# Kernel optimization log

Hardware: AMD Instinct MI355X
Metric: run time of the kernel (lower is better)

The kernel has to match this reference:

```python
import jax, jax.numpy as jnp
import numpy as np

BETA = 0.25      # commitment loss weight
DECAY = 0.99     # EMA decay
EPS = 1e-5       # Laplace smoothing for counts


def setup_inputs() -> dict:
    key = jax.random.key(0)
    k1, k2, k3 = jax.random.split(key, 3)
    B, d, h, w, K = 16, 64, 64, 64, 1024
    z_e = jax.random.normal(k1, (B, d, h, w), dtype=jnp.float32)
    codebook = jax.random.normal(k2, (K, d), dtype=jnp.float32)
    ema_count = jnp.ones((K,), dtype=jnp.float32)
    ema_sum = jax.random.normal(k3, (K, d), dtype=jnp.float32)
    return {"z_e": z_e, "codebook": codebook, "ema_count": ema_count, "ema_sum": ema_sum}


def reference(z_e, codebook, ema_count, ema_sum):
    B, d, h, w = z_e.shape
    K = codebook.shape[0]
    # [B,d,h,w] -> [N,d], N = B*h*w
    z_flat = jnp.transpose(z_e, (0, 2, 3, 1)).reshape(-1, d)
    # squared euclidean distances [N,K]
    dist = (jnp.sum(z_flat * z_flat, axis=1, keepdims=True)
            - 2.0 * (z_flat @ codebook.T)
            + jnp.sum(codebook * codebook, axis=1)[None, :])
    indices = jnp.argmin(dist, axis=1)                      # [N] int
    e_k = codebook[indices].reshape(B, h, w, d).transpose(0, 3, 1, 2)  # [B,d,h,w]

    # --- EMA codebook update (training mode, no grad) ---
    zf = jax.lax.stop_gradient(z_flat)
    counts = jax.ops.segment_sum(jnp.ones((zf.shape[0],), dtype=zf.dtype), indices, num_segments=K)
    sums = jax.ops.segment_sum(zf, indices, num_segments=K)
    new_count = ema_count * DECAY + (1.0 - DECAY) * counts
    new_sum = ema_sum * DECAY + (1.0 - DECAY) * sums
    n = jnp.sum(new_count)
    count_s = (new_count + EPS) / (n + K * EPS) * n
    new_codebook = new_sum / count_s[:, None]

    # straight-through estimator
    e_k_ste = z_e + jax.lax.stop_gradient(e_k - z_e)
    L_commit = (jnp.mean((z_e - jax.lax.stop_gradient(e_k)) ** 2)
                + BETA * jnp.mean((jax.lax.stop_gradient(z_e) - e_k) ** 2))
    return (e_k_ste, indices.reshape(B, h, w), L_commit, new_codebook, new_count, new_sum)
```

## Files before the change

### kernel.cpp

```cpp
#include <hip/hip_runtime.h>
#include <hip/hip_bf16.h>
#include <hip/hip_fp16.h>

#define NB 16
#define DD 64
#define HW 4096
#define NTOT 65536
#define KC 1024

#define O_EK   0
#define O_IDX  4194304
#define O_L    4259840
#define O_CB   4259841
#define O_CNT  4325377
#define O_SUM  4326401

#define WS_IDX    0
#define WS_LCPART 65536
#define WS_N      66048
#define WS_CNORM  66560
#define WS_PSUM   67584
#define WS_PCNT   329728
#define WS_CBH    399360
#define WS_CBL    432128

typedef _Float16 v8h __attribute__((ext_vector_type(8)));
typedef float    v4f __attribute__((ext_vector_type(4)));
typedef unsigned short ush;

__global__ __launch_bounds__(256) void k_pre(const float* __restrict__ cb,
                                             const float* __restrict__ ema_count,
                                             float* __restrict__ cnorm,
                                             float* __restrict__ n_ws,
                                             unsigned short* __restrict__ cbh,
                                             unsigned short* __restrict__ cbl) {
    const int t = threadIdx.x;
    const int w = (blockIdx.x * 256 + t) >> 6;
    const int l = t & 63;
    float s = 0.f;
    if (l < 16) {
        float4 v = *(const float4*)(cb + (size_t)w * DD + l * 4);
        s = v.x * v.x + v.y * v.y + v.z * v.z + v.w * v.w;
    }
#pragma unroll
    for (int m = 1; m <= 8; m <<= 1) s += __shfl_xor(s, m, 64);
    if (l == 0) cnorm[w] = s;

    const int e4 = blockIdx.x * 256 + t;
    if (e4 < 16384) {
        float4 v4 = ((const float4*)cb)[e4];
        __half hx = __float2half(v4.x), hy = __float2half(v4.y),
               hz = __float2half(v4.z), hw2 = __float2half(v4.w);
        ushort4 h4 = { __half_as_ushort(hx), __half_as_ushort(hy),
                       __half_as_ushort(hz), __half_as_ushort(hw2) };
        ((ushort4*)cbh)[e4] = h4;
        ushort4 l4 = { __half_as_ushort(__float2half(v4.x - __half2float(hx))),
                       __half_as_ushort(__float2half(v4.y - __half2float(hy))),
                       __half_as_ushort(__float2half(v4.z - __half2float(hz))),
                       __half_as_ushort(__float2half(v4.w - __half2float(hw2))) };
        ((ushort4*)cbl)[e4] = l4;
    }

    if (blockIdx.x == 0) {
        __shared__ float red[256];
        red[t] = ema_count[t] + ema_count[t + 256] + ema_count[t + 512] + ema_count[t + 768];
        __syncthreads();
        for (int s2 = 128; s2 >= 1; s2 >>= 1) {
            if (t < s2) red[t] += red[t + s2];
            __syncthreads();
        }
        if (t == 0) n_ws[0] = 0.99f * red[0] + 0.01f * 65536.0f;
    }
}

__global__ __launch_bounds__(512) void k_argmin(const float* __restrict__ z_e,
                                                const float* __restrict__ cbf,
                                                const unsigned short* __restrict__ cbh,
                                                const unsigned short* __restrict__ cbl,
                                                const float* __restrict__ cnorm,
                                                int* __restrict__ idx_ws,
                                                float* __restrict__ out) {
    __shared__ __align__(16) unsigned char ldsAB[32768];
    __shared__ __align__(16) float slab[2048];
    __shared__ int idx_lds[128];
    __shared__ int flagrows[128];
    __shared__ int flagi1[128];
    __shared__ int flagi2[128];
    __shared__ int nflag;

    ush (*A2h)[128][8]  = (ush(*)[128][8])(ldsAB);
    ush (*A2l)[128][8]  = (ush(*)[128][8])(ldsAB + 16384);
    ush (*B2h)[8][64][8] = (ush(*)[8][64][8])(ldsAB);
    ush (*B2l)[8][64][8] = (ush(*)[8][64][8])(ldsAB + 16384);

    const int t  = threadIdx.x;
    const int n0 = blockIdx.x * 128;
    const int bb  = n0 >> 12;
    const int hw0 = n0 & 4095;
    const float* zbase = z_e + (size_t)bb * (DD * HW) + hw0;

    if (t == 0) nflag = 0;

    {
        const int jr   = t >> 5;
        const int m4   = (t & 31) << 2;
        const int chl  = t >> 8;
        const int cm   = t & 127;
        const int half = (t >> 7) & 1;
        for (int sl = 0; sl < 4; ++sl) {
            if (sl) __syncthreads();
            float4 v = *(const float4*)(zbase + (size_t)(sl * 16 + jr) * HW + m4);
            *(float4*)&slab[jr * 128 + m4] = v;
            __syncthreads();
            unsigned hv[2], lv[2];
#pragma unroll
            for (int p = 0; p < 2; ++p) {
                int jj = chl * 8 + half * 4 + p * 2;
                float v0 = slab[jj * 128 + cm];
                float v1 = slab[(jj + 1) * 128 + cm];
                __half h0 = __float2half(v0), h1 = __float2half(v1);
                __half l0 = __float2half(v0 - __half2float(h0));
                __half l1 = __float2half(v1 - __half2float(h1));
                hv[p] = (unsigned)__half_as_ushort(h0) | ((unsigned)__half_as_ushort(h1) << 16);
                lv[p] = (unsigned)__half_as_ushort(l0) | ((unsigned)__half_as_ushort(l1) << 16);
            }
            uint2 hq = {hv[0], hv[1]}, lq = {lv[0], lv[1]};
            *(uint2*)&A2h[sl * 2 + chl][cm][half * 4] = hq;
            *(uint2*)&A2l[sl * 2 + chl][cm][half * 4] = lq;
        }
    }
    __syncthreads();

    const int w    = t >> 6;
    const int lane = t & 63;
    const int c    = lane & 15;
    const int q    = lane >> 4;

    v8h Afh[2], Afl[2];
    {
        int m = 16 * w + c;
#pragma unroll
        for (int s = 0; s < 2; ++s) {
            Afh[s] = *(const v8h*)&A2h[s * 4 + q][m][0];
            Afl[s] = *(const v8h*)&A2l[s * 4 + q][m][0];
        }
    }
    __syncthreads();

    const int ch0   = t >> 6;
    const int code0 = t & 63;

    {
        size_t g0 = ((size_t)code0) * 64 + ch0 * 8;
        *(uint4*)&B2h[0][ch0][code0][0] = *(const uint4*)(cbh + g0);
        *(uint4*)&B2l[0][ch0][code0][0] = *(const uint4*)(cbl + g0);
    }
    __syncthreads();

    float m1f[4], m2f[4];
#pragma unroll
    for (int r = 0; r < 4; ++r) { m1f[r] = 3.4e38f; m2f[r] = 3.4e38f; }

    for (int kt = 0; kt < 16; ++kt) {
        const int cur = kt & 1, nxt = cur ^ 1;
        uint4 ph0, pl0;
        if (kt < 15) {
            size_t g0 = ((size_t)((kt + 1) * 64 + code0)) * 64 + ch0 * 8;
            ph0 = *(const uint4*)(cbh + g0);
            pl0 = *(const uint4*)(cbl + g0);
        }

#pragma unroll
        for (int sub = 0; sub < 4; ++sub) {
            const int cl = sub * 16 + c;
            v8h Bfh0 = *(const v8h*)&B2h[cur][q][cl][0];
            v8h Bfh1 = *(const v8h*)&B2h[cur][4 + q][cl][0];
            v8h Bfl0 = *(const v8h*)&B2l[cur][q][cl][0];
            v8h Bfl1 = *(const v8h*)&B2l[cur][4 + q][cl][0];
            const unsigned kg = (unsigned)(kt * 64 + cl);
            float cnc = cnorm[kg];
            v4f acc = {0.f, 0.f, 0.f, 0.f};
            acc = __builtin_amdgcn_mfma_f32_16x16x32_f16(Afh[0], Bfh0, acc, 0, 0, 0);
            acc = __builtin_amdgcn_mfma_f32_16x16x32_f16(Afh[1], Bfh1, acc, 0, 0, 0);
            acc = __builtin_amdgcn_mfma_f32_16x16x32_f16(Afh[0], Bfl0, acc, 0, 0, 0);
            acc = __builtin_amdgcn_mfma_f32_16x16x32_f16(Afh[1], Bfl1, acc, 0, 0, 0);
            acc = __builtin_amdgcn_mfma_f32_16x16x32_f16(Afl[0], Bfh0, acc, 0, 0, 0);
            acc = __builtin_amdgcn_mfma_f32_16x16x32_f16(Afl[1], Bfh1, acc, 0, 0, 0);
#pragma unroll
            for (int r = 0; r < 4; ++r) {
                float v = fmaf(-2.0f, acc[r], cnc);
                unsigned vu = (__float_as_uint(v) & 0xFFFFFC00u) | kg;
                float vp = __uint_as_float(vu);
                m2f[r] = fminf(m2f[r], fmaxf(m1f[r], vp));
                m1f[r] = fminf(m1f[r], vp);
            }
        }

        if (kt < 15) {
            *(uint4*)&B2h[nxt][ch0][code0][0] = ph0;
            *(uint4*)&B2l[nxt][ch0][code0][0] = pl0;
        }
        __syncthreads();
    }

#pragma unroll
    for (int r = 0; r < 4; ++r) {
        float a = m1f[r], b2 = m2f[r];
#pragma unroll
        for (int mask = 1; mask <= 8; mask <<= 1) {
            float o1 = __shfl_xor(a, mask, 64);
            float o2 = __shfl_xor(b2, mask, 64);
            float mx = fmaxf(a, o1);
            a  = fminf(a, o1);
            b2 = fminf(fminf(b2, o2), mx);
        }
        if (c == 0) {
            int row = 16 * w + q * 4 + r;
            int i1 = (int)(__float_as_uint(a) & 1023u);
            idx_lds[row] = i1;
            float margin = fmaf(fabsf(a), 6e-4f, 0.0015f);
            if (b2 - a < margin) {
                int p = atomicAdd(&nflag, 1);
                flagrows[p] = row;
                flagi1[p] = i1;
                flagi2[p] = (int)(__float_as_uint(b2) & 1023u);
            }
        }
    }
    __syncthreads();

    {
        int nf = nflag;
        for (int f = w; f < nf; f += 8) {
            int row = flagrows[f], i1 = flagi1[f], i2x = flagi2[f];
            const float* zrow = zbase + row;
            float zj = zrow[(size_t)lane * HW];
            float p1 = zj * cbf[(size_t)i1  * DD + lane];
            float p2 = zj * cbf[(size_t)i2x * DD + lane];
#pragma unroll
            for (int mask = 1; mask <= 32; mask <<= 1) {
                p1 += __shfl_xor(p1, mask, 64);
                p2 += __shfl_xor(p2, mask, 64);
            }
            if (lane == 0) {
                float d1 = fmaf(-2.0f, p1, cnorm[i1]);
                float d2 = fmaf(-2.0f, p2, cnorm[i2x]);
                if (d2 < d1 || (d2 == d1 && i2x < i1)) idx_lds[row] = i2x;
            }
        }
    }
    __syncthreads();

    if (t < 128) {
        int bi = idx_lds[t];
        out[O_IDX + n0 + t] = (float)bi;
        idx_ws[n0 + t] = bi;
    }
}

__global__ __launch_bounds__(1024) void k_out(const int* __restrict__ idx_ws,
                                              const float* __restrict__ z_e,
                                              const float* __restrict__ cb,
                                              float* __restrict__ psum,
                                              int* __restrict__ pcnt,
                                              float* __restrict__ lc_part,
                                              float* __restrict__ out) {
    __shared__ float acc[KC];
    __shared__ int bins[KC];
    __shared__ float cbj[KC];
    __shared__ float lcr[16];
    const int j = blockIdx.x & 63;
    const int c = blockIdx.x >> 6;
    const int t = threadIdx.x;
    acc[t] = 0.f;
    bins[t] = 0;
    cbj[t] = cb[(size_t)t * DD + j];
    __syncthreads();
    const float* zj = z_e + (size_t)j * HW;
    float* oj = out + O_EK + (size_t)j * HW;
    const int base = c * 16384;
    float lc = 0.f;
#pragma unroll
    for (int i = 0; i < 4; ++i) {
        int n4 = base + i * 4096 + t * 4;
        int b = n4 >> 12, hw = n4 & 4095;
        size_t zoff = (size_t)b * (DD * HW) + hw;
        float4 z4 = *(const float4*)(zj + zoff);
        int4   k4 = *(const int4*)(idx_ws + n4);
        float e0 = cbj[k4.x], e1 = cbj[k4.y], e2 = cbj[k4.z], e3 = cbj[k4.w];
        float4 o4 = { z4.x + (e0 - z4.x), z4.y + (e1 - z4.y),
                      z4.z + (e2 - z4.z), z4.w + (e3 - z4.w) };
        *(float4*)(oj + zoff) = o4;
        float d0 = z4.x - e0, d1 = z4.y - e1, d2 = z4.z - e2, d3 = z4.w - e3;
        lc = fmaf(d0, d0, lc); lc = fmaf(d1, d1, lc);
        lc = fmaf(d2, d2, lc); lc = fmaf(d3, d3, lc);
        atomicAdd(&acc[k4.x], z4.x);
        atomicAdd(&acc[k4.y], z4.y);
        atomicAdd(&acc[k4.z], z4.z);
        atomicAdd(&acc[k4.w], z4.w);
        if (j == 0) {
            atomicAdd(&bins[k4.x], 1); atomicAdd(&bins[k4.y], 1);
            atomicAdd(&bins[k4.z], 1); atomicAdd(&bins[k4.w], 1);
        }
    }
    __syncthreads();
    psum[(size_t)c * 65536 + j * 1024 + t] = acc[t];
    if (j == 0) pcnt[c * 1024 + t] = bins[t];
#pragma unroll
    for (int m = 32; m >= 1; m >>= 1) lc += __shfl_xor(lc, m, 64);
    if ((t & 63) == 0) lcr[t >> 6] = lc;
    __syncthreads();
    if (t == 0) {
        float s = 0.f;
#pragma unroll
        for (int u = 0; u < 16; ++u) s += lcr[u];
        lc_part[blockIdx.x] = s;
    }
}

__global__ __launch_bounds__(1024) void k_epi(const float* __restrict__ psum,
                                              const int* __restrict__ pcnt,
                                              const float* __restrict__ ema_sum,
                                              const float* __restrict__ ema_count,
                                              const float* __restrict__ n_ws,
                                              const float* __restrict__ lc_part,
                                              float* __restrict__ out) {
    const int t = threadIdx.x;
    const int e = blockIdx.x * 1024 + t;
    const int k = e >> 6, j = e & 63;
    float s4 = psum[j * 1024 + k] + psum[65536 + j * 1024 + k]
             + psum[131072 + j * 1024 + k] + psum[196608 + j * 1024 + k];
    float ns = ema_sum[e] * 0.99f + 0.01f * s4;
    out[O_SUM + e] = ns;
    int cnt = pcnt[k] + pcnt[1024 + k] + pcnt[2048 + k] + pcnt[3072 + k];
    float nc = ema_count[k] * 0.99f + 0.01f * (float)cnt;
    float n  = n_ws[0];
    float cs = (nc + 1e-5f) / (n + 1024.0f * 1e-5f) * n;
    out[O_CB + e] = ns / cs;
    if (blockIdx.x == 0) {
        int c2 = pcnt[t] + pcnt[1024 + t] + pcnt[2048 + t] + pcnt[3072 + t];
        out[O_CNT + t] = ema_count[t] * 0.99f + 0.01f * (float)c2;
    }
    if (blockIdx.x == 1) {
        __shared__ float red[512];
        if (t < 512) red[t] = (t < 256) ? lc_part[t] : 0.f;
        __syncthreads();
        for (int s = 256; s >= 1; s >>= 1) {
            if (t < s) red[t] += red[t + s];
            __syncthreads();
        }
        if (t == 0) out[O_L] = 1.25f * red[0] * (1.0f / 4194304.0f);
    }
}

extern "C" void kernel_launch(void* const* d_in, const int* in_sizes, int n_in,
                              void* d_out, int out_size, void* d_ws, size_t ws_size,
                              hipStream_t stream) {
    const float* z_e       = (const float*)d_in[0];
    const float* cb        = (const float*)d_in[1];
    const float* ema_count = (const float*)d_in[2];
    const float* ema_sum   = (const float*)d_in[3];
    float* out             = (float*)d_out;

    float* ws_f      = (float*)d_ws;
    int*   idx_ws    = (int*)d_ws;
    float* lc_part   = ws_f + WS_LCPART;
    float* n_ws      = ws_f + WS_N;
    float* cnorm_ws  = ws_f + WS_CNORM;
    float* psum      = ws_f + WS_PSUM;
    int*   pcnt      = (int*)(ws_f + WS_PCNT);
    unsigned short* cbh = (unsigned short*)(ws_f + WS_CBH);
    unsigned short* cbl = (unsigned short*)(ws_f + WS_CBL);

    k_pre<<<256, 256, 0, stream>>>(cb, ema_count, cnorm_ws, n_ws, cbh, cbl);
    k_argmin<<<NTOT / 128, 512, 0, stream>>>(z_e, cb, cbh, cbl, cnorm_ws, idx_ws, out);
    k_out<<<256, 1024, 0, stream>>>(idx_ws, z_e, cb, psum, pcnt, lc_part, out);
    k_epi<<<64, 1024, 0, stream>>>(psum, pcnt, ema_sum, ema_count, n_ws, lc_part, out);
}
```

Before: 139.1 us.

## Shrink argmin blocks to two waves with two row-tiles per wave

The argmin kernel now uses 128-thread blocks covering 64 rows. Each wave computes two 16-row tiles, so every codebook B fragment read from LDS is reused twice, and the six MFMAs are split into two independent accumulator chains to expose ILP. The slab buffer is aliased into the shared LDS region, lowering LDS per block so more blocks can be resident. Indices are passed to k_out as 16-bit values to cut workspace traffic, but each block now loads the full codebook tile with fewer threads.

```diff
diff --git a/kernel.cpp b/kernel.cpp
--- a/kernel.cpp
+++ b/kernel.cpp
@@ -73,28 +73,28 @@
     }
 }
 
-__global__ __launch_bounds__(512) void k_argmin(const float* __restrict__ z_e,
-                                                const float* __restrict__ cbf,
-                                                const unsigned short* __restrict__ cbh,
-                                                const unsigned short* __restrict__ cbl,
-                                                const float* __restrict__ cnorm,
-                                                int* __restrict__ idx_ws,
-                                                float* __restrict__ out) {
+__global__ __launch_bounds__(128, 2) void k_argmin(const float* __restrict__ z_e,
+                                                   const float* __restrict__ cbf,
+                                                   const unsigned short* __restrict__ cbh,
+                                                   const unsigned short* __restrict__ cbl,
+                                                   const float* __restrict__ cnorm,
+                                                   unsigned short* __restrict__ idx16,
+                                                   float* __restrict__ out) {
     __shared__ __align__(16) unsigned char ldsAB[32768];
-    __shared__ __align__(16) float slab[2048];
-    __shared__ int idx_lds[128];
-    __shared__ int flagrows[128];
-    __shared__ int flagi1[128];
-    __shared__ int flagi2[128];
+    __shared__ int idx_lds[64];
+    __shared__ int flagrows[64];
+    __shared__ int flagi1[64];
+    __shared__ int flagi2[64];
     __shared__ int nflag;
 
-    ush (*A2h)[128][8]  = (ush(*)[128][8])(ldsAB);
-    ush (*A2l)[128][8]  = (ush(*)[128][8])(ldsAB + 16384);
+    ush (*A2h)[64][8] = (ush(*)[64][8])(ldsAB);
+    ush (*A2l)[64][8] = (ush(*)[64][8])(ldsAB + 8192);
+    float* slab = (float*)(ldsAB + 16384);
     ush (*B2h)[8][64][8] = (ush(*)[8][64][8])(ldsAB);
     ush (*B2l)[8][64][8] = (ush(*)[8][64][8])(ldsAB + 16384);
 
     const int t  = threadIdx.x;
-    const int n0 = blockIdx.x * 128;
+    const int n0 = blockIdx.x * 64;
     const int bb  = n0 >> 12;
     const int hw0 = n0 & 4095;
     const float* zbase = z_e + (size_t)bb * (DD * HW) + hw0;
@@ -102,31 +102,37 @@
     if (t == 0) nflag = 0;
 
     {
-        const int jr   = t >> 5;
-        const int m4   = (t & 31) << 2;
-        const int chl  = t >> 8;
-        const int cm   = t & 127;
-        const int half = (t >> 7) & 1;
+        const int m  = t & 63;
+        const int ps = t >> 6;
         for (int sl = 0; sl < 4; ++sl) {
             if (sl) __syncthreads();
-            float4 v = *(const float4*)(zbase + (size_t)(sl * 16 + jr) * HW + m4);
-            *(float4*)&slab[jr * 128 + m4] = v;
+#pragma unroll
+            for (int p = 0; p < 2; ++p) {
+                int fidx = t + p * 128;
+                int jl   = fidx >> 4;
+                int m4   = (fidx & 15) << 2;
+                float4 v = *(const float4*)(zbase + (size_t)(sl * 16 + jl) * HW + m4);
+                *(float4*)&slab[jl * 64 + m4] = v;
+            }
             __syncthreads();
-            unsigned hv[2], lv[2];
-#pragma unroll
-            for (int p = 0; p < 2; ++p) {
-                int jj = chl * 8 + half * 4 + p * 2;
-                float v0 = slab[jj * 128 + cm];
-                float v1 = slab[(jj + 1) * 128 + cm];
-                __half h0 = __float2half(v0), h1 = __float2half(v1);
-                __half l0 = __float2half(v0 - __half2float(h0));
-                __half l1 = __float2half(v1 - __half2float(h1));
-                hv[p] = (unsigned)__half_as_ushort(h0) | ((unsigned)__half_as_ushort(h1) << 16);
-                lv[p] = (unsigned)__half_as_ushort(l0) | ((unsigned)__half_as_ushort(l1) << 16);
-            }
-            uint2 hq = {hv[0], hv[1]}, lq = {lv[0], lv[1]};
-            *(uint2*)&A2h[sl * 2 + chl][cm][half * 4] = hq;
-            *(uint2*)&A2l[sl * 2 + chl][cm][half * 4] = lq;
+#pragma unroll
+            for (int chl = 0; chl < 2; ++chl) {
+                unsigned hv[2], lv[2];
+#pragma unroll
+                for (int pp = 0; pp < 2; ++pp) {
+                    int jl = chl * 8 + ps * 4 + pp * 2;
+                    float v0 = slab[jl * 64 + m];
+                    float v1 = slab[(jl + 1) * 64 + m];
+                    __half h0 = __float2half(v0), h1 = __float2half(v1);
+                    __half l0 = __float2half(v0 - __half2float(h0));
+                    __half l1 = __float2half(v1 - __half2float(h1));
+                    hv[pp] = (unsigned)__half_as_ushort(h0) | ((unsigned)__half_as_ushort(h1) << 16);
+                    lv[pp] = (unsigned)__half_as_ushort(l0) | ((unsigned)__half_as_ushort(l1) << 16);
+                }
+                uint2 hq = {hv[0], hv[1]}, lq = {lv[0], lv[1]};
+                *(uint2*)&A2h[sl * 2 + chl][m][ps * 4] = hq;
+                *(uint2*)&A2l[sl * 2 + chl][m][ps * 4] = lq;
+            }
         }
     }
     __syncthreads();
@@ -136,38 +142,47 @@
     const int c    = lane & 15;
     const int q    = lane >> 4;
 
-    v8h Afh[2], Afl[2];
-    {
-        int m = 16 * w + c;
+    v8h Afh[2][2], Afl[2][2];
+#pragma unroll
+    for (int g = 0; g < 2; ++g) {
+        int m = 32 * w + 16 * g + c;
 #pragma unroll
         for (int s = 0; s < 2; ++s) {
-            Afh[s] = *(const v8h*)&A2h[s * 4 + q][m][0];
-            Afl[s] = *(const v8h*)&A2l[s * 4 + q][m][0];
-        }
-    }
-    __syncthreads();
-
-    const int ch0   = t >> 6;
+            Afh[g][s] = *(const v8h*)&A2h[s * 4 + q][m][0];
+            Afl[g][s] = *(const v8h*)&A2l[s * 4 + q][m][0];
+        }
+    }
+    __syncthreads();
+
     const int code0 = t & 63;
-
-    {
-        size_t g0 = ((size_t)code0) * 64 + ch0 * 8;
-        *(uint4*)&B2h[0][ch0][code0][0] = *(const uint4*)(cbh + g0);
-        *(uint4*)&B2l[0][ch0][code0][0] = *(const uint4*)(cbl + g0);
-    }
-    __syncthreads();
-
-    float m1f[4], m2f[4];
-#pragma unroll
-    for (int r = 0; r < 4; ++r) { m1f[r] = 3.4e38f; m2f[r] = 3.4e38f; }
+    const int cb0   = t >> 6;
+
+#pragma unroll
+    for (int u = 0; u < 4; ++u) {
+        int ch = cb0 + u * 2;
+        size_t g0 = ((size_t)code0) * 64 + ch * 8;
+        *(uint4*)&B2h[0][ch][code0][0] = *(const uint4*)(cbh + g0);
+        *(uint4*)&B2l[0][ch][code0][0] = *(const uint4*)(cbl + g0);
+    }
+    __syncthreads();
+
+    float m1f[2][4], m2f[2][4];
+#pragma unroll
+    for (int g = 0; g < 2; ++g)
+#pragma unroll
+        for (int r = 0; r < 4; ++r) { m1f[g][r] = 3.4e38f; m2f[g][r] = 3.4e38f; }
 
     for (int kt = 0; kt < 16; ++kt) {
         const int cur = kt & 1, nxt = cur ^ 1;
-        uint4 ph0, pl0;
+        uint4 ph[4], pl[4];
         if (kt < 15) {
-            size_t g0 = ((size_t)((kt + 1) * 64 + code0)) * 64 + ch0 * 8;
-            ph0 = *(const uint4*)(cbh + g0);
-            pl0 = *(const uint4*)(cbl + g0);
+#pragma unroll
+            for (int u = 0; u < 4; ++u) {
+                int ch = cb0 + u * 2;
+                size_t g0 = ((size_t)((kt + 1) * 64 + code0)) * 64 + ch * 8;
+                ph[u] = *(const uint4*)(cbh + g0);
+                pl[u] = *(const uint4*)(cbl + g0);
+            }
         }
 
 #pragma unroll
@@ -179,59 +194,69 @@
             v8h Bfl1 = *(const v8h*)&B2l[cur][4 + q][cl][0];
             const unsigned kg = (unsigned)(kt * 64 + cl);
             float cnc = cnorm[kg];
-            v4f acc = {0.f, 0.f, 0.f, 0.f};
-            acc = __builtin_amdgcn_mfma_f32_16x16x32_f16(Afh[0], Bfh0, acc, 0, 0, 0);
-            acc = __builtin_amdgcn_mfma_f32_16x16x32_f16(Afh[1], Bfh1, acc, 0, 0, 0);
-            acc = __builtin_amdgcn_mfma_f32_16x16x32_f16(Afh[0], Bfl0, acc, 0, 0, 0);
-            acc = __builtin_amdgcn_mfma_f32_16x16x32_f16(Afh[1], Bfl1, acc, 0, 0, 0);
-            acc = __builtin_amdgcn_mfma_f32_16x16x32_f16(Afl[0], Bfh0, acc, 0, 0, 0);
-            acc = __builtin_amdgcn_mfma_f32_16x16x32_f16(Afl[1], Bfh1, acc, 0, 0, 0);
-#pragma unroll
-            for (int r = 0; r < 4; ++r) {
-                float v = fmaf(-2.0f, acc[r], cnc);
-                unsigned vu = (__float_as_uint(v) & 0xFFFFFC00u) | kg;
-                float vp = __uint_as_float(vu);
-                m2f[r] = fminf(m2f[r], fmaxf(m1f[r], vp));
-                m1f[r] = fminf(m1f[r], vp);
+#pragma unroll
+            for (int g = 0; g < 2; ++g) {
+                v4f accA = {0.f, 0.f, 0.f, 0.f};
+                v4f accB = {0.f, 0.f, 0.f, 0.f};
+                accA = __builtin_amdgcn_mfma_f32_16x16x32_f16(Afh[g][0], Bfh0, accA, 0, 0, 0);
+                accB = __builtin_amdgcn_mfma_f32_16x16x32_f16(Afh[g][1], Bfh1, accB, 0, 0, 0);
+                accA = __builtin_amdgcn_mfma_f32_16x16x32_f16(Afh[g][0], Bfl0, accA, 0, 0, 0);
+                accB = __builtin_amdgcn_mfma_f32_16x16x32_f16(Afh[g][1], Bfl1, accB, 0, 0, 0);
+                accA = __builtin_amdgcn_mfma_f32_16x16x32_f16(Afl[g][0], Bfh0, accA, 0, 0, 0);
+                accB = __builtin_amdgcn_mfma_f32_16x16x32_f16(Afl[g][1], Bfh1, accB, 0, 0, 0);
+#pragma unroll
+                for (int r = 0; r < 4; ++r) {
+                    float v = fmaf(-2.0f, accA[r] + accB[r], cnc);
+                    unsigned vu = (__float_as_uint(v) & 0xFFFFFC00u) | kg;
+                    float vp = __uint_as_float(vu);
+                    m2f[g][r] = fminf(m2f[g][r], fmaxf(m1f[g][r], vp));
+                    m1f[g][r] = fminf(m1f[g][r], vp);
+                }
             }
         }
 
         if (kt < 15) {
-            *(uint4*)&B2h[nxt][ch0][code0][0] = ph0;
-            *(uint4*)&B2l[nxt][ch0][code0][0] = pl0;
+#pragma unroll
+            for (int u = 0; u < 4; ++u) {
+                int ch = cb0 + u * 2;
+                *(uint4*)&B2h[nxt][ch][code0][0] = ph[u];
+                *(uint4*)&B2l[nxt][ch][code0][0] = pl[u];
+            }
         }
         __syncthreads();
     }
 
 #pragma unroll
-    for (int r = 0; r < 4; ++r) {
-        float a = m1f[r], b2 = m2f[r];
-#pragma unroll
-        for (int mask = 1; mask <= 8; mask <<= 1) {
-            float o1 = __shfl_xor(a, mask, 64);
-            float o2 = __shfl_xor(b2, mask, 64);
-            float mx = fmaxf(a, o1);
-            a  = fminf(a, o1);
-            b2 = fminf(fminf(b2, o2), mx);
-        }
-        if (c == 0) {
-            int row = 16 * w + q * 4 + r;
-            int i1 = (int)(__float_as_uint(a) & 1023u);
-            idx_lds[row] = i1;
-            float margin = fmaf(fabsf(a), 6e-4f, 0.0015f);
-            if (b2 - a < margin) {
-                int p = atomicAdd(&nflag, 1);
-                flagrows[p] = row;
-                flagi1[p] = i1;
-                flagi2[p] = (int)(__float_as_uint(b2) & 1023u);
-            }
-        }
-    }
+    for (int g = 0; g < 2; ++g)
+#pragma unroll
+        for (int r = 0; r < 4; ++r) {
+            float a = m1f[g][r], b2 = m2f[g][r];
+#pragma unroll
+            for (int mask = 1; mask <= 8; mask <<= 1) {
+                float o1 = __shfl_xor(a, mask, 64);
+                float o2 = __shfl_xor(b2, mask, 64);
+                float mx = fmaxf(a, o1);
+                a  = fminf(a, o1);
+                b2 = fminf(fminf(b2, o2), mx);
+            }
+            if (c == 0) {
+                int row = 32 * w + 16 * g + q * 4 + r;
+                int i1 = (int)(__float_as_uint(a) & 1023u);
+                idx_lds[row] = i1;
+                float margin = fmaf(fabsf(a), 6e-4f, 0.0015f);
+                if (b2 - a < margin) {
+                    int p = atomicAdd(&nflag, 1);
+                    flagrows[p] = row;
+                    flagi1[p] = i1;
+                    flagi2[p] = (int)(__float_as_uint(b2) & 1023u);
+                }
+            }
+        }
     __syncthreads();
 
     {
         int nf = nflag;
-        for (int f = w; f < nf; f += 8) {
+        for (int f = w; f < nf; f += 2) {
             int row = flagrows[f], i1 = flagi1[f], i2x = flagi2[f];
             const float* zrow = zbase + row;
             float zj = zrow[(size_t)lane * HW];
@@ -251,14 +276,14 @@
     }
     __syncthreads();
 
-    if (t < 128) {
+    if (t < 64) {
         int bi = idx_lds[t];
         out[O_IDX + n0 + t] = (float)bi;
-        idx_ws[n0 + t] = bi;
+        idx16[n0 + t] = (unsigned short)bi;
     }
 }
 
-__global__ __launch_bounds__(1024) void k_out(const int* __restrict__ idx_ws,
+__global__ __launch_bounds__(1024) void k_out(const unsigned short* __restrict__ idx16,
                                               const float* __restrict__ z_e,
                                               const float* __restrict__ cb,
                                               float* __restrict__ psum,
@@ -286,7 +311,7 @@
         int b = n4 >> 12, hw = n4 & 4095;
         size_t zoff = (size_t)b * (DD * HW) + hw;
         float4 z4 = *(const float4*)(zj + zoff);
-        int4   k4 = *(const int4*)(idx_ws + n4);
+        ushort4 k4 = *(const ushort4*)(idx16 + n4);
         float e0 = cbj[k4.x], e1 = cbj[k4.y], e2 = cbj[k4.z], e3 = cbj[k4.w];
         float4 o4 = { z4.x + (e0 - z4.x), z4.y + (e1 - z4.y),
                       z4.z + (e2 - z4.z), z4.w + (e3 - z4.w) };
@@ -363,7 +388,7 @@
     float* out             = (float*)d_out;
 
     float* ws_f      = (float*)d_ws;
-    int*   idx_ws    = (int*)d_ws;
+    unsigned short* idx16 = (unsigned short*)d_ws;
     float* lc_part   = ws_f + WS_LCPART;
     float* n_ws      = ws_f + WS_N;
     float* cnorm_ws  = ws_f + WS_CNORM;
@@ -373,7 +398,7 @@
     unsigned short* cbl = (unsigned short*)(ws_f + WS_CBL);
 
     k_pre<<<256, 256, 0, stream>>>(cb, ema_count, cnorm_ws, n_ws, cbh, cbl);
-    k_argmin<<<NTOT / 128, 512, 0, stream>>>(z_e, cb, cbh, cbl, cnorm_ws, idx_ws, out);
-    k_out<<<256, 1024, 0, stream>>>(idx_ws, z_e, cb, psum, pcnt, lc_part, out);
+    k_argmin<<<NTOT / 64, 128, 0, stream>>>(z_e, cb, cbh, cbl, cnorm_ws, idx16, out);
+    k_out<<<256, 1024, 0, stream>>>(idx16, z_e, cb, psum, pcnt, lc_part, out);
     k_epi<<<64, 1024, 0, stream>>>(psum, pcnt, ema_sum, ema_count, n_ws, lc_part, out);
 }
```

Measured after the change: 143.9 us. 3.5% more time.

## Restructure argmin to 128-thread blocks streaming pre-swizzled codebook from global

Applied to the files above, without the earlier changes.

The argmin kernel now uses 2 waves per 128-row block, and each wave holds 64 rows of A fragments in registers (4 groups). B fragments are read straight from a pre-swizzled global codebook with register double-buffering, which removes the LDS staging and per-tile barriers. The -2 scale is folded into the codebook split and cnorm seeds the accumulator, using two independent accumulator chains. Indices are stored as 16-bit to shrink traffic into k_out. This costs more registers, lower occupancy (launch_bounds 128,1), and relies on L2/cache to serve repeated codebook reads.

```diff
diff --git a/kernel.cpp b/kernel.cpp
--- a/kernel.cpp
+++ b/kernel.cpp
@@ -49,16 +49,20 @@
     const int e4 = blockIdx.x * 256 + t;
     if (e4 < 16384) {
         float4 v4 = ((const float4*)cb)[e4];
-        __half hx = __float2half(v4.x), hy = __float2half(v4.y),
-               hz = __float2half(v4.z), hw2 = __float2half(v4.w);
+        float sx = -2.f * v4.x, sy = -2.f * v4.y, sz = -2.f * v4.z, sw = -2.f * v4.w;
+        __half hx = __float2half(sx), hy = __float2half(sy),
+               hz = __float2half(sz), hw2 = __float2half(sw);
         ushort4 h4 = { __half_as_ushort(hx), __half_as_ushort(hy),
                        __half_as_ushort(hz), __half_as_ushort(hw2) };
-        ((ushort4*)cbh)[e4] = h4;
-        ushort4 l4 = { __half_as_ushort(__float2half(v4.x - __half2float(hx))),
-                       __half_as_ushort(__float2half(v4.y - __half2float(hy))),
-                       __half_as_ushort(__float2half(v4.z - __half2float(hz))),
-                       __half_as_ushort(__float2half(v4.w - __half2float(hw2))) };
-        ((ushort4*)cbl)[e4] = l4;
+        ushort4 l4 = { __half_as_ushort(__float2half(sx - __half2float(hx))),
+                       __half_as_ushort(__float2half(sy - __half2float(hy))),
+                       __half_as_ushort(__float2half(sz - __half2float(hz))),
+                       __half_as_ushort(__float2half(sw - __half2float(hw2))) };
+        const int code = e4 >> 4, f4 = e4 & 15;
+        const int chunk = f4 >> 1, half = f4 & 1;
+        const int o4 = ((code >> 4) * 8 + chunk) * 32 + (code & 15) * 2 + half;
+        ((ushort4*)cbh)[o4] = h4;
+        ((ushort4*)cbl)[o4] = l4;
     }
 
     if (blockIdx.x == 0) {
@@ -73,26 +77,22 @@
     }
 }
 
-__global__ __launch_bounds__(512) void k_argmin(const float* __restrict__ z_e,
-                                                const float* __restrict__ cbf,
-                                                const unsigned short* __restrict__ cbh,
-                                                const unsigned short* __restrict__ cbl,
-                                                const float* __restrict__ cnorm,
-                                                int* __restrict__ idx_ws,
-                                                float* __restrict__ out) {
-    __shared__ __align__(16) unsigned char ldsAB[32768];
-    __shared__ __align__(16) float slab[2048];
+__global__ __launch_bounds__(128, 1) void k_argmin(const float* __restrict__ z_e,
+                                                   const float* __restrict__ cbf,
+                                                   const unsigned short* __restrict__ cbh,
+                                                   const unsigned short* __restrict__ cbl,
+                                                   const float* __restrict__ cnorm,
+                                                   unsigned short* __restrict__ idx16,
+                                                   float* __restrict__ out) {
+    __shared__ __align__(16) ush A2h[8][128][8];
+    __shared__ __align__(16) ush A2l[8][128][8];
+    __shared__ __align__(16) float slab[8][128];
     __shared__ int idx_lds[128];
     __shared__ int flagrows[128];
     __shared__ int flagi1[128];
     __shared__ int flagi2[128];
     __shared__ int nflag;
 
-    ush (*A2h)[128][8]  = (ush(*)[128][8])(ldsAB);
-    ush (*A2l)[128][8]  = (ush(*)[128][8])(ldsAB + 16384);
-    ush (*B2h)[8][64][8] = (ush(*)[8][64][8])(ldsAB);
-    ush (*B2l)[8][64][8] = (ush(*)[8][64][8])(ldsAB + 16384);
-
     const int t  = threadIdx.x;
     const int n0 = blockIdx.x * 128;
     const int bb  = n0 >> 12;
@@ -101,33 +101,32 @@
 
     if (t == 0) nflag = 0;
 
-    {
-        const int jr   = t >> 5;
-        const int m4   = (t & 31) << 2;
-        const int chl  = t >> 8;
-        const int cm   = t & 127;
-        const int half = (t >> 7) & 1;
-        for (int sl = 0; sl < 4; ++sl) {
-            if (sl) __syncthreads();
-            float4 v = *(const float4*)(zbase + (size_t)(sl * 16 + jr) * HW + m4);
-            *(float4*)&slab[jr * 128 + m4] = v;
-            __syncthreads();
-            unsigned hv[2], lv[2];
-#pragma unroll
-            for (int p = 0; p < 2; ++p) {
-                int jj = chl * 8 + half * 4 + p * 2;
-                float v0 = slab[jj * 128 + cm];
-                float v1 = slab[(jj + 1) * 128 + cm];
-                __half h0 = __float2half(v0), h1 = __float2half(v1);
-                __half l0 = __float2half(v0 - __half2float(h0));
-                __half l1 = __float2half(v1 - __half2float(h1));
-                hv[p] = (unsigned)__half_as_ushort(h0) | ((unsigned)__half_as_ushort(h1) << 16);
-                lv[p] = (unsigned)__half_as_ushort(l0) | ((unsigned)__half_as_ushort(l1) << 16);
-            }
-            uint2 hq = {hv[0], hv[1]}, lq = {lv[0], lv[1]};
-            *(uint2*)&A2h[sl * 2 + chl][cm][half * 4] = hq;
-            *(uint2*)&A2l[sl * 2 + chl][cm][half * 4] = lq;
-        }
+    for (int sl = 0; sl < 8; ++sl) {
+        if (sl) __syncthreads();
+#pragma unroll
+        for (int p = 0; p < 2; ++p) {
+            int fidx = t + p * 128;
+            int jl   = fidx >> 5;
+            int m4   = (fidx & 31) << 2;
+            float4 v = *(const float4*)(zbase + (size_t)(sl * 8 + jl) * HW + m4);
+            *(float4*)&slab[jl][m4] = v;
+        }
+        __syncthreads();
+        unsigned hv[4], lv[4];
+#pragma unroll
+        for (int p = 0; p < 4; ++p) {
+            float v0 = slab[2 * p][t];
+            float v1 = slab[2 * p + 1][t];
+            __half h0 = __float2half(v0), h1 = __float2half(v1);
+            __half l0 = __float2half(v0 - __half2float(h0));
+            __half l1 = __float2half(v1 - __half2float(h1));
+            hv[p] = (unsigned)__half_as_ushort(h0) | ((unsigned)__half_as_ushort(h1) << 16);
+            lv[p] = (unsigned)__half_as_ushort(l0) | ((unsigned)__half_as_ushort(l1) << 16);
+        }
+        uint4 hq = {hv[0], hv[1], hv[2], hv[3]};
+        uint4 lq = {lv[0], lv[1], lv[2], lv[3]};
+        *(uint4*)&A2h[sl][t][0] = hq;
+        *(uint4*)&A2l[sl][t][0] = lq;
     }
     __syncthreads();
 
@@ -136,102 +135,98 @@
     const int c    = lane & 15;
     const int q    = lane >> 4;
 
-    v8h Afh[2], Afl[2];
-    {
-        int m = 16 * w + c;
+    v8h Afh[4][2], Afl[4][2];
+#pragma unroll
+    for (int g = 0; g < 4; ++g) {
+        int m = 64 * w + 16 * g + c;
 #pragma unroll
         for (int s = 0; s < 2; ++s) {
-            Afh[s] = *(const v8h*)&A2h[s * 4 + q][m][0];
-            Afl[s] = *(const v8h*)&A2l[s * 4 + q][m][0];
-        }
-    }
-    __syncthreads();
-
-    const int ch0   = t >> 6;
-    const int code0 = t & 63;
-
-    {
-        size_t g0 = ((size_t)code0) * 64 + ch0 * 8;
-        *(uint4*)&B2h[0][ch0][code0][0] = *(const uint4*)(cbh + g0);
-        *(uint4*)&B2l[0][ch0][code0][0] = *(const uint4*)(cbl + g0);
-    }
-    __syncthreads();
-
-    float m1f[4], m2f[4];
-#pragma unroll
-    for (int r = 0; r < 4; ++r) { m1f[r] = 3.4e38f; m2f[r] = 3.4e38f; }
-
-    for (int kt = 0; kt < 16; ++kt) {
-        const int cur = kt & 1, nxt = cur ^ 1;
-        uint4 ph0, pl0;
-        if (kt < 15) {
-            size_t g0 = ((size_t)((kt + 1) * 64 + code0)) * 64 + ch0 * 8;
-            ph0 = *(const uint4*)(cbh + g0);
-            pl0 = *(const uint4*)(cbl + g0);
-        }
-
-#pragma unroll
-        for (int sub = 0; sub < 4; ++sub) {
-            const int cl = sub * 16 + c;
-            v8h Bfh0 = *(const v8h*)&B2h[cur][q][cl][0];
-            v8h Bfh1 = *(const v8h*)&B2h[cur][4 + q][cl][0];
-            v8h Bfl0 = *(const v8h*)&B2l[cur][q][cl][0];
-            v8h Bfl1 = *(const v8h*)&B2l[cur][4 + q][cl][0];
-            const unsigned kg = (unsigned)(kt * 64 + cl);
-            float cnc = cnorm[kg];
-            v4f acc = {0.f, 0.f, 0.f, 0.f};
-            acc = __builtin_amdgcn_mfma_f32_16x16x32_f16(Afh[0], Bfh0, acc, 0, 0, 0);
-            acc = __builtin_amdgcn_mfma_f32_16x16x32_f16(Afh[1], Bfh1, acc, 0, 0, 0);
-            acc = __builtin_amdgcn_mfma_f32_16x16x32_f16(Afh[0], Bfl0, acc, 0, 0, 0);
-            acc = __builtin_amdgcn_mfma_f32_16x16x32_f16(Afh[1], Bfl1, acc, 0, 0, 0);
-            acc = __builtin_amdgcn_mfma_f32_16x16x32_f16(Afl[0], Bfh0, acc, 0, 0, 0);
-            acc = __builtin_amdgcn_mfma_f32_16x16x32_f16(Afl[1], Bfh1, acc, 0, 0, 0);
-#pragma unroll
-            for (int r = 0; r < 4; ++r) {
-                float v = fmaf(-2.0f, acc[r], cnc);
-                unsigned vu = (__float_as_uint(v) & 0xFFFFFC00u) | kg;
-                float vp = __uint_as_float(vu);
-                m2f[r] = fminf(m2f[r], fmaxf(m1f[r], vp));
-                m1f[r] = fminf(m1f[r], vp);
+            Afh[g][s] = *(const v8h*)&A2h[s * 4 + q][m][0];
+            Afl[g][s] = *(const v8h*)&A2l[s * 4 + q][m][0];
+        }
+    }
+
+    const ush* bh = cbh + q * 128 + c * 8;
+    const ush* bl = cbl + q * 128 + c * 8;
+
+    float m1f[4][4], m2f[4][4];
+#pragma unroll
+    for (int g = 0; g < 4; ++g)
+#pragma unroll
+        for (int r = 0; r < 4; ++r) { m1f[g][r] = 3.4e38f; m2f[g][r] = 3.4e38f; }
+
+#define LOADB(H0, H1, L0, L1, u) {                      \
+        size_t o = (size_t)(u) * 1024;                  \
+        H0 = *(const v8h*)(bh + o);                     \
+        H1 = *(const v8h*)(bh + o + 512);               \
+        L0 = *(const v8h*)(bl + o);                     \
+        L1 = *(const v8h*)(bl + o + 512); }
+
+#define COMPUTE(H0, H1, L0, L1, u) {                                            \
+        const unsigned kg = (unsigned)((u) * 16 + c);                           \
+        const float cnc = cnorm[kg];                                            \
+        _Pragma("unroll")                                                       \
+        for (int g = 0; g < 4; ++g) {                                           \
+            v4f accA = {cnc, cnc, cnc, cnc};                                    \
+            v4f accB = {0.f, 0.f, 0.f, 0.f};                                    \
+            accA = __builtin_amdgcn_mfma_f32_16x16x32_f16(Afh[g][0], H0, accA, 0, 0, 0); \
+            accB = __builtin_amdgcn_mfma_f32_16x16x32_f16(Afh[g][1], H1, accB, 0, 0, 0); \
+            accA = __builtin_amdgcn_mfma_f32_16x16x32_f16(Afh[g][0], L0, accA, 0, 0, 0); \
+            accB = __builtin_amdgcn_mfma_f32_16x16x32_f16(Afh[g][1], L1, accB, 0, 0, 0); \
+            accA = __builtin_amdgcn_mfma_f32_16x16x32_f16(Afl[g][0], H0, accA, 0, 0, 0); \
+            accB = __builtin_amdgcn_mfma_f32_16x16x32_f16(Afl[g][1], H1, accB, 0, 0, 0); \
+            _Pragma("unroll")                                                   \
+            for (int r = 0; r < 4; ++r) {                                       \
+                float v = accA[r] + accB[r];                                    \
+                unsigned vu = (__float_as_uint(v) & 0xFFFFFC00u) | kg;          \
+                float vp = __uint_as_float(vu);                                 \
+                m2f[g][r] = fminf(m2f[g][r], fmaxf(m1f[g][r], vp));             \
+                m1f[g][r] = fminf(m1f[g][r], vp);                               \
+            }                                                                   \
+        } }
+
+    v8h Ah0, Ah1, Al0, Al1, Bh0, Bh1, Bl0, Bl1;
+    LOADB(Ah0, Ah1, Al0, Al1, 0);
+    for (int u = 0; u < 64; u += 2) {
+        LOADB(Bh0, Bh1, Bl0, Bl1, u + 1);
+        COMPUTE(Ah0, Ah1, Al0, Al1, u);
+        if (u + 2 < 64) LOADB(Ah0, Ah1, Al0, Al1, u + 2);
+        COMPUTE(Bh0, Bh1, Bl0, Bl1, u + 1);
+    }
+#undef LOADB
+#undef COMPUTE
+
+#pragma unroll
+    for (int g = 0; g < 4; ++g)
+#pragma unroll
+        for (int r = 0; r < 4; ++r) {
+            float a = m1f[g][r], b2 = m2f[g][r];
+#pragma unroll
+            for (int mask = 1; mask <= 8; mask <<= 1) {
+                float o1 = __shfl_xor(a, mask, 64);
+                float o2 = __shfl_xor(b2, mask, 64);
+                float mx = fmaxf(a, o1);
+                a  = fminf(a, o1);
+                b2 = fminf(fminf(b2, o2), mx);
             }
-        }
-
-        if (kt < 15) {
-            *(uint4*)&B2h[nxt][ch0][code0][0] = ph0;
-            *(uint4*)&B2l[nxt][ch0][code0][0] = pl0;
-        }
-        __syncthreads();
-    }
-
-#pragma unroll
-    for (int r = 0; r < 4; ++r) {
-        float a = m1f[r], b2 = m2f[r];
-#pragma unroll
-        for (int mask = 1; mask <= 8; mask <<= 1) {
-            float o1 = __shfl_xor(a, mask, 64);
-            float o2 = __shfl_xor(b2, mask, 64);
-            float mx = fmaxf(a, o1);
-            a  = fminf(a, o1);
-            b2 = fminf(fminf(b2, o2), mx);
-        }
-        if (c == 0) {
-            int row = 16 * w + q * 4 + r;
-            int i1 = (int)(__float_as_uint(a) & 1023u);
-            idx_lds[row] = i1;
-            float margin = fmaf(fabsf(a), 6e-4f, 0.0015f);
-            if (b2 - a < margin) {
-                int p = atomicAdd(&nflag, 1);
-                flagrows[p] = row;
-                flagi1[p] = i1;
-                flagi2[p] = (int)(__float_as_uint(b2) & 1023u);
+            if (c == 0) {
+                int row = 64 * w + 16 * g + q * 4 + r;
+                int i1 = (int)(__float_as_uint(a) & 1023u);
+                idx_lds[row] = i1;
+                float margin = fmaf(fabsf(a), 6e-4f, 0.0015f);
+                if (b2 - a < margin) {
+                    int p = atomicAdd(&nflag, 1);
+                    flagrows[p] = row;
+                    flagi1[p] = i1;
+                    flagi2[p] = (int)(__float_as_uint(b2) & 1023u);
+                }
             }
         }
-    }
     __syncthreads();
 
     {
         int nf = nflag;
-        for (int f = w; f < nf; f += 8) {
+        for (int f = w; f < nf; f += 2) {
             int row = flagrows[f], i1 = flagi1[f], i2x = flagi2[f];
             const float* zrow = zbase + row;
             float zj = zrow[(size_t)lane * HW];
@@ -254,11 +249,11 @@
     if (t < 128) {
         int bi = idx_lds[t];
         out[O_IDX + n0 + t] = (float)bi;
-        idx_ws[n0 + t] = bi;
-    }
-}
-
-__global__ __launch_bounds__(1024) void k_out(const int* __restrict__ idx_ws,
+        idx16[n0 + t] = (unsigned short)bi;
+    }
+}
+
+__global__ __launch_bounds__(1024) void k_out(const unsigned short* __restrict__ idx16,
                                               const float* __restrict__ z_e,
                                               const float* __restrict__ cb,
                                               float* __restrict__ psum,
@@ -286,7 +281,7 @@
         int b = n4 >> 12, hw = n4 & 4095;
         size_t zoff = (size_t)b * (DD * HW) + hw;
         float4 z4 = *(const float4*)(zj + zoff);
-        int4   k4 = *(const int4*)(idx_ws + n4);
+        ushort4 k4 = *(const ushort4*)(idx16 + n4);
         float e0 = cbj[k4.x], e1 = cbj[k4.y], e2 = cbj[k4.z], e3 = cbj[k4.w];
         float4 o4 = { z4.x + (e0 - z4.x), z4.y + (e1 - z4.y),
                       z4.z + (e2 - z4.z), z4.w + (e3 - z4.w) };
@@ -363,7 +358,7 @@
     float* out             = (float*)d_out;
 
     float* ws_f      = (float*)d_ws;
-    int*   idx_ws    = (int*)d_ws;
+    unsigned short* idx16 = (unsigned short*)d_ws;
     float* lc_part   = ws_f + WS_LCPART;
     float* n_ws      = ws_f + WS_N;
     float* cnorm_ws  = ws_f + WS_CNORM;
@@ -373,7 +368,7 @@
     unsigned short* cbl = (unsigned short*)(ws_f + WS_CBL);
 
     k_pre<<<256, 256, 0, stream>>>(cb, ema_count, cnorm_ws, n_ws, cbh, cbl);
-    k_argmin<<<NTOT / 128, 512, 0, stream>>>(z_e, cb, cbh, cbl, cnorm_ws, idx_ws, out);
-    k_out<<<256, 1024, 0, stream>>>(idx_ws, z_e, cb, psum, pcnt, lc_part, out);
+    k_argmin<<<NTOT / 128, 128, 0, stream>>>(z_e, cb, cbh, cbl, cnorm_ws, idx16, out);
+    k_out<<<256, 1024, 0, stream>>>(idx16, z_e, cb, psum, pcnt, lc_part, out);
     k_epi<<<64, 1024, 0, stream>>>(psum, pcnt, ema_sum, ema_count, n_ws, lc_part, out);
 }
```

Result: slower. 162.4 us (+16.7%).
